# Performance work log

Measured on AMD Instinct MI355X. Metric: run time of the kernel, lower is better.

The kernel has to match this reference:

```python
import jax, jax.numpy as jnp
import numpy as np

VOCAB = 32000
EMBED = 512
HIDDEN = 512
SEQ = 4096


def setup_inputs() -> dict:
    key = jax.random.key(0)
    ks = jax.random.split(key, 20)
    s = 1.0 / np.sqrt(HIDDEN)

    def n(k, shape):
        return (jax.random.normal(k, shape, dtype=jnp.float32) * s).astype(jnp.float32)

    inp = {}
    inp["input"] = jax.random.randint(ks[0], (SEQ,), 0, VOCAB)
    inp["embed_w"] = n(ks[1], (VOCAB, EMBED))
    # layer 0 (input size EMBED), forward and backward directions; gate order i,f,g,o
    inp["Wih0f"] = n(ks[2], (4 * HIDDEN, EMBED))
    inp["Whh0f"] = n(ks[3], (4 * HIDDEN, HIDDEN))
    inp["b0f"] = n(ks[4], (4 * HIDDEN,))  # b_ih + b_hh combined (same math)
    inp["Wih0b"] = n(ks[5], (4 * HIDDEN, EMBED))
    inp["Whh0b"] = n(ks[6], (4 * HIDDEN, HIDDEN))
    inp["b0b"] = n(ks[7], (4 * HIDDEN,))
    # layer 1 (input size 2*HIDDEN)
    inp["Wih1f"] = n(ks[8], (4 * HIDDEN, 2 * HIDDEN))
    inp["Whh1f"] = n(ks[9], (4 * HIDDEN, HIDDEN))
    inp["b1f"] = n(ks[10], (4 * HIDDEN,))
    inp["Wih1b"] = n(ks[11], (4 * HIDDEN, 2 * HIDDEN))
    inp["Whh1b"] = n(ks[12], (4 * HIDDEN, HIDDEN))
    inp["b1b"] = n(ks[13], (4 * HIDDEN,))
    # output head
    inp["Wlin"] = n(ks[14], (VOCAB, 2 * HIDDEN))
    inp["blin"] = n(ks[15], (VOCAB,))
    return inp


def _lstm_dir(xproj, Whh, reverse):
    # xproj: [S, 4H] = x @ Wih.T + b, precomputed outside the scan.
    H = Whh.shape[1]
    WhhT = Whh.T  # [H, 4H]

    def step(carry, xp):
        h, c = carry
        g = xp + h @ WhhT  # [4H]
        i, f, gg, o = jnp.split(g, 4)
        i = jax.nn.sigmoid(i)
        f = jax.nn.sigmoid(f)
        gg = jnp.tanh(gg)
        o = jax.nn.sigmoid(o)
        c = f * c + i * gg
        h = o * jnp.tanh(c)
        return (h, c), h

    h0 = jnp.zeros((H,), xproj.dtype)
    _, hs = jax.lax.scan(step, (h0, h0), xproj, reverse=reverse)
    return hs  # [S, H], aligned to original time order


def _bilstm_layer(x, Wihf, Whhf, bf, Wihb, Whhb, bb):
    hf = _lstm_dir(x @ Wihf.T + bf, Whhf, reverse=False)
    hb = _lstm_dir(x @ Wihb.T + bb, Whhb, reverse=True)
    return jnp.concatenate([hf, hb], axis=-1)  # [S, 2H]


def reference(input, embed_w, Wih0f, Whh0f, b0f, Wih0b, Whh0b, b0b,
              Wih1f, Whh1f, b1f, Wih1b, Whh1b, b1b, Wlin, blin):
    x = embed_w[input]  # [S, E]  (batch=1 squeezed away; same math)
    x = _bilstm_layer(x, Wih0f, Whh0f, b0f, Wih0b, Whh0b, b0b)
    x = _bilstm_layer(x, Wih1f, Whh1f, b1f, Wih1b, Whh1b, b1b)
    out = x @ Wlin.T + blin  # [S, VOCAB]
    return out
```

## Files before the change

### kernel.cpp

```cpp
#include <hip/hip_runtime.h>
#include <hip/hip_bf16.h>
#include <stdint.h>

#define S_LEN 4096

typedef __attribute__((ext_vector_type(8))) short short8;
typedef __attribute__((ext_vector_type(4))) float f32x4;

__device__ inline unsigned short f2bf(float f) {
  unsigned int x = __float_as_uint(f);
  x += 0x7fffu + ((x >> 16) & 1u);
  return (unsigned short)(x >> 16);
}

__device__ inline float sigm(float x) { return 1.0f / (1.0f + __expf(-x)); }
__device__ inline float tanhf_(float x) {
  float e = __expf(-2.0f * fabsf(x));
  float t = (1.0f - e) / (1.0f + e);
  return copysignf(t, x);
}

__device__ inline void gload_lds16(const void* g, void* l) {
  __builtin_amdgcn_global_load_lds(
      (const __attribute__((address_space(1))) unsigned int*)g,
      (__attribute__((address_space(3))) unsigned int*)l, 16, 0, 0);
}

__global__ void embed_kernel(const int* __restrict__ idx, const float* __restrict__ E,
                             unsigned short* __restrict__ x0b) {
  const int row = blockIdx.x;
  const int t = threadIdx.x;
  const int id = idx[row];
  f32x4 v = ((const f32x4*)(E + (size_t)id * 512))[t];
  ushort4 u;
  u.x = f2bf(v[0]); u.y = f2bf(v[1]); u.z = f2bf(v[2]); u.w = f2bf(v[3]);
  ((ushort4*)(x0b + (size_t)row * 512))[t] = u;
}

__global__ void f32_to_bf16_kernel(const float* __restrict__ src, unsigned short* __restrict__ dst) {
  const size_t i = (size_t)blockIdx.x * blockDim.x + threadIdx.x;
  f32x4 v = ((const f32x4*)src)[i];
  ushort4 u;
  u.x = f2bf(v[0]); u.y = f2bf(v[1]); u.z = f2bf(v[2]); u.w = f2bf(v[3]);
  ((ushort4*)dst)[i] = u;
}

template <bool BF32>
__global__ __launch_bounds__(256) void gemm_bt(
    const unsigned short* __restrict__ A,
    const void* __restrict__ Bsrc,
    const float* __restrict__ bias,
    float* __restrict__ C,
    int M, int N, int K)
{
  __shared__ unsigned short Al[128 * 32];
  __shared__ unsigned short Bl[128 * 32];
  const int tiles_n = N >> 7;
  const int tm = (blockIdx.x / tiles_n) << 7;
  const int tn = (blockIdx.x % tiles_n) << 7;
  const int t = threadIdx.x;
  const int w = t >> 6, l = t & 63;
  const int wr = w >> 1, wc = w & 1;

  f32x4 acc[4][4] = {};

  for (int k0 = 0; k0 < K; k0 += 32) {
    __syncthreads();
    {
      const int rb = w * 32;
      const unsigned short* ga = A + (size_t)(tm + rb + (l >> 2)) * K + k0 + (l & 3) * 8;
      gload_lds16(ga, &Al[rb * 32]);
      gload_lds16(ga + (size_t)16 * K, &Al[(rb + 16) * 32]);
    }
    if constexpr (!BF32) {
      const unsigned short* B = (const unsigned short*)Bsrc;
      const int rb = w * 32;
      const unsigned short* gb = B + (size_t)(tn + rb + (l >> 2)) * K + k0 + (l & 3) * 8;
      gload_lds16(gb, &Bl[rb * 32]);
      gload_lds16(gb + (size_t)16 * K, &Bl[(rb + 16) * 32]);
    } else {
      const float* B = (const float*)Bsrc;
      const int row = t >> 1, half = t & 1;
      const f32x4* src = (const f32x4*)(B + (size_t)(tn + row) * K + k0 + half * 16);
      f32x4 v0 = src[0], v1 = src[1], v2 = src[2], v3 = src[3];
      short8 p0, p1;
      p0[0] = f2bf(v0[0]); p0[1] = f2bf(v0[1]); p0[2] = f2bf(v0[2]); p0[3] = f2bf(v0[3]);
      p0[4] = f2bf(v1[0]); p0[5] = f2bf(v1[1]); p0[6] = f2bf(v1[2]); p0[7] = f2bf(v1[3]);
      p1[0] = f2bf(v2[0]); p1[1] = f2bf(v2[1]); p1[2] = f2bf(v2[2]); p1[3] = f2bf(v2[3]);
      p1[4] = f2bf(v3[0]); p1[5] = f2bf(v3[1]); p1[6] = f2bf(v3[2]); p1[7] = f2bf(v3[3]);
      *(short8*)&Bl[row * 32 + half * 16] = p0;
      *(short8*)&Bl[row * 32 + half * 16 + 8] = p1;
    }
    __syncthreads();

    const int lrow = l & 15;
    const int lkb = (l >> 4) * 8;
    short8 af[4], bfr[4];
    #pragma unroll
    for (int fm = 0; fm < 4; fm++)
      af[fm] = *(const short8*)&Al[(wr * 64 + fm * 16 + lrow) * 32 + lkb];
    #pragma unroll
    for (int fn = 0; fn < 4; fn++)
      bfr[fn] = *(const short8*)&Bl[(wc * 64 + fn * 16 + lrow) * 32 + lkb];
    #pragma unroll
    for (int fm = 0; fm < 4; fm++)
      #pragma unroll
      for (int fn = 0; fn < 4; fn++)
        acc[fm][fn] = __builtin_amdgcn_mfma_f32_16x16x32_bf16(af[fm], bfr[fn], acc[fm][fn], 0, 0, 0);
  }

  const int r0 = tm + wr * 64;
  const int c0 = tn + wc * 64 + (l & 15);
  const int rbase = (l >> 4) * 4;
  #pragma unroll
  for (int fm = 0; fm < 4; fm++) {
    #pragma unroll
    for (int fn = 0; fn < 4; fn++) {
      const int col = c0 + fn * 16;
      const float bv = bias ? bias[col] : 0.0f;
      #pragma unroll
      for (int rg = 0; rg < 4; rg++) {
        const int rr = r0 + fm * 16 + rbase + rg;
        C[(size_t)rr * N + col] = acc[fm][fn][rg] + bv;
      }
    }
  }
}

__global__ __launch_bounds__(512, 1) void lstm_layer(
    const float* __restrict__ WhhF, const float* __restrict__ WhhB,
    const float* __restrict__ biasF, const float* __restrict__ biasB,
    const float* __restrict__ xproj,
    unsigned int* __restrict__ Hx,
    unsigned short* __restrict__ Hb)
{
  const int S = S_LEN;
  const int dir = blockIdx.x & 1;
  const int chunk = blockIdx.x >> 1;
  const float* Whh = dir ? WhhB : WhhF;
  const float* bias = dir ? biasB : biasF;
  const int t = threadIdx.x;
  const int w = t >> 6, l = t & 63;
  const int g = l >> 4;
  const int jl = (l >> 3) & 1;
  const int o = l & 7;
  const int elem = w * 2 + jl;
  const int r = g * 512 + chunk * 16 + elem;
  const int xoff = dir * 2048, hoff = dir * 512;

  f32x4 wv[16];
  {
    const f32x4* wp = (const f32x4*)(Whh + (size_t)r * 512 + o * 64);
    #pragma unroll
    for (int i = 0; i < 16; i++) {
      asm volatile("global_load_dwordx4 %0, %1, off\n\ts_waitcnt vmcnt(0)"
                   : "=v"(wv[i]) : "v"(wp + i) : "memory");
    }
  }
  const float bv = bias[r];

  __shared__ float hsh[2][8 * 68];
  float c = 0.0f;
  const int slot = (t >> 6) * 68 + (t & 63);

  float xp_cur = 0.0f;
  if (o == 0) {
    const int t0 = dir ? (S - 1) : 0;
    xp_cur = xproj[(size_t)t0 * 4096 + xoff + r] + bv;
  }

  for (int st = 0; st < S; st++) {
    const int tcur = dir ? (S - 1 - st) : st;
    const int pp = st & 1;

    float xp_nxt = 0.0f;
    if (o == 0 && st + 1 < S) {
      const int tn = dir ? (S - 2 - st) : (st + 1);
      xp_nxt = xproj[(size_t)tn * 4096 + xoff + r] + bv;
    }

    if (st == 0) {
      hsh[0][slot] = 0.0f;
    } else {
      const int tprev = dir ? (tcur + 1) : (tcur - 1);
      const unsigned int* src = Hx + (size_t)tprev * 1024 + hoff + t;
      unsigned int v;
      int cap = 1 << 16;
      do {
        v = __hip_atomic_load(src, __ATOMIC_RELAXED, __HIP_MEMORY_SCOPE_AGENT);
      } while (v == 0xFFFFFFFFu && --cap > 0);
      hsh[pp][slot] = __uint_as_float(v);
    }
    __syncthreads();

    float acc = 0.0f;
    const f32x4* hp = (const f32x4*)&hsh[pp][o * 68];
    #pragma unroll
    for (int i = 0; i < 16; i++) {
      f32x4 h4 = hp[i];
      acc = fmaf(wv[i][0], h4[0], acc);
      acc = fmaf(wv[i][1], h4[1], acc);
      acc = fmaf(wv[i][2], h4[2], acc);
      acc = fmaf(wv[i][3], h4[3], acc);
    }
    acc += __shfl_xor(acc, 1);
    acc += __shfl_xor(acc, 2);
    acc += __shfl_xor(acc, 4);
    acc += xp_cur;

    const float av = (g == 2) ? tanhf_(acc) : sigm(acc);
    const float f_ = __shfl(av, (l & 8) + 16);
    const float g_ = __shfl(av, (l & 8) + 32);
    const float o_ = __shfl(av, (l & 8) + 48);

    if ((l & 55) == 0) {
      c = f_ * c + av * g_;
      const float h = o_ * tanhf_(c);
      const size_t ofs = (size_t)tcur * 1024 + hoff + chunk * 16 + elem;
      __hip_atomic_store(Hx + ofs, __float_as_uint(h),
                         __ATOMIC_RELAXED, __HIP_MEMORY_SCOPE_AGENT);
      Hb[ofs] = f2bf(h);
    }
    xp_cur = xp_nxt;
  }
}

extern "C" void kernel_launch(void* const* d_in, const int* in_sizes, int n_in,
                              void* d_out, int out_size, void* d_ws, size_t ws_size,
                              hipStream_t stream) {
  (void)in_sizes; (void)n_in; (void)out_size; (void)ws_size;
  const int*   input   = (const int*)d_in[0];
  const float* embed_w = (const float*)d_in[1];
  const float* Wih0f   = (const float*)d_in[2];
  const float* Whh0f   = (const float*)d_in[3];
  const float* b0f     = (const float*)d_in[4];
  const float* Wih0b   = (const float*)d_in[5];
  const float* Whh0b   = (const float*)d_in[6];
  const float* b0b     = (const float*)d_in[7];
  const float* Wih1f   = (const float*)d_in[8];
  const float* Whh1f   = (const float*)d_in[9];
  const float* b1f     = (const float*)d_in[10];
  const float* Wih1b   = (const float*)d_in[11];
  const float* Whh1b   = (const float*)d_in[12];
  const float* b1b     = (const float*)d_in[13];
  const float* Wlin    = (const float*)d_in[14];
  const float* blin    = (const float*)d_in[15];

  char* ws = (char*)d_ws;
  unsigned short* x0b   = (unsigned short*)(ws);
  unsigned short* Wih0  = (unsigned short*)(ws + ((size_t)4  << 20));
  unsigned short* Wih1  = (unsigned short*)(ws + ((size_t)8  << 20));
  unsigned short* H0b   = (unsigned short*)(ws + ((size_t)16 << 20));
  unsigned short* H1b   = (unsigned short*)(ws + ((size_t)24 << 20));

  float* dout  = (float*)d_out;
  float* xproj = dout;
  unsigned int* H0 = (unsigned int*)(dout + ((size_t)16 << 20));
  unsigned int* H1 = (unsigned int*)(dout + ((size_t)20 << 20));

  hipMemsetAsync(H0, 0xFF, (size_t)8 * 1024 * 1024 * 4, stream);

  embed_kernel<<<4096, 128, 0, stream>>>(input, embed_w, x0b);

  f32_to_bf16_kernel<<<1024, 256, 0, stream>>>(Wih0f, Wih0);
  f32_to_bf16_kernel<<<1024, 256, 0, stream>>>(Wih0b, Wih0 + (size_t)2048 * 512);
  f32_to_bf16_kernel<<<2048, 256, 0, stream>>>(Wih1f, Wih1);
  f32_to_bf16_kernel<<<2048, 256, 0, stream>>>(Wih1b, Wih1 + (size_t)2048 * 1024);

  gemm_bt<false><<<32 * 32, 256, 0, stream>>>(x0b, Wih0, nullptr, xproj, 4096, 4096, 512);
  lstm_layer<<<64, 512, 0, stream>>>(Whh0f, Whh0b, b0f, b0b, xproj, H0, H0b);

  gemm_bt<false><<<32 * 32, 256, 0, stream>>>(H0b, Wih1, nullptr, xproj, 4096, 4096, 1024);
  lstm_layer<<<64, 512, 0, stream>>>(Whh1f, Whh1b, b1f, b1b, xproj, H1, H1b);

  gemm_bt<true><<<32 * 250, 256, 0, stream>>>(H1b, Wlin, blin, dout, 4096, 32000, 1024);
}
```

Baseline: 12.00 ms.

## Stream bf16 recurrent weights from cache each step and pack h exchanges into 64-bit words

Recurrent weights are converted to bf16 once up front, and the LSTM kernel now reloads them from global memory/cache on every timestep instead of holding 64 fp32 values per thread in registers. The hidden-state exchange between blocks uses 64-bit atomic loads and stores covering two elements, which halves the polling and store traffic, and every lane now computes the cell update. This cuts register pressure but adds a per-step weight reload on the serial recurrence path and lowers the precision of the recurrent weights.

```diff
diff --git a/kernel.cpp b/kernel.cpp
--- a/kernel.cpp
+++ b/kernel.cpp
@@ -5,12 +5,17 @@
 #define S_LEN 4096
 
 typedef __attribute__((ext_vector_type(8))) short short8;
+typedef __attribute__((ext_vector_type(8))) unsigned short ushort8;
 typedef __attribute__((ext_vector_type(4))) float f32x4;
+typedef __attribute__((ext_vector_type(2))) float f32x2;
 
 __device__ inline unsigned short f2bf(float f) {
   unsigned int x = __float_as_uint(f);
   x += 0x7fffu + ((x >> 16) & 1u);
   return (unsigned short)(x >> 16);
+}
+__device__ inline float bf2f(unsigned short u) {
+  return __uint_as_float(((unsigned int)u) << 16);
 }
 
 __device__ inline float sigm(float x) { return 1.0f / (1.0f + __expf(-x)); }
@@ -128,7 +133,8 @@
 }
 
 __global__ __launch_bounds__(512, 1) void lstm_layer(
-    const float* __restrict__ WhhF, const float* __restrict__ WhhB,
+    const unsigned short* __restrict__ WhhBf16F,
+    const unsigned short* __restrict__ WhhBf16B,
     const float* __restrict__ biasF, const float* __restrict__ biasB,
     const float* __restrict__ xproj,
     unsigned int* __restrict__ Hx,
@@ -137,7 +143,7 @@
   const int S = S_LEN;
   const int dir = blockIdx.x & 1;
   const int chunk = blockIdx.x >> 1;
-  const float* Whh = dir ? WhhB : WhhF;
+  const unsigned short* Whh = dir ? WhhBf16B : WhhBf16F;
   const float* bias = dir ? biasB : biasF;
   const int t = threadIdx.x;
   const int w = t >> 6, l = t & 63;
@@ -148,20 +154,12 @@
   const int r = g * 512 + chunk * 16 + elem;
   const int xoff = dir * 2048, hoff = dir * 512;
 
-  f32x4 wv[16];
-  {
-    const f32x4* wp = (const f32x4*)(Whh + (size_t)r * 512 + o * 64);
-    #pragma unroll
-    for (int i = 0; i < 16; i++) {
-      asm volatile("global_load_dwordx4 %0, %1, off\n\ts_waitcnt vmcnt(0)"
-                   : "=v"(wv[i]) : "v"(wp + i) : "memory");
-    }
-  }
+  const ushort8* wp = (const ushort8*)(Whh + (size_t)r * 512 + o * 64);
   const float bv = bias[r];
 
   __shared__ float hsh[2][8 * 68];
   float c = 0.0f;
-  const int slot = (t >> 6) * 68 + (t & 63);
+  const int slot2 = (t >> 5) * 68 + ((2 * t) & 63);
 
   float xp_cur = 0.0f;
   if (o == 0) {
@@ -173,6 +171,10 @@
     const int tcur = dir ? (S - 1 - st) : st;
     const int pp = st & 1;
 
+    ushort8 wv[8];
+    #pragma unroll
+    for (int j = 0; j < 8; j++) wv[j] = wp[j];
+
     float xp_nxt = 0.0f;
     if (o == 0 && st + 1 < S) {
       const int tn = dir ? (S - 2 - st) : (st + 1);
@@ -180,28 +182,32 @@
     }
 
     if (st == 0) {
-      hsh[0][slot] = 0.0f;
-    } else {
+      if (t < 256) *(f32x2*)&hsh[0][slot2] = f32x2{0.0f, 0.0f};
+    } else if (t < 256) {
       const int tprev = dir ? (tcur + 1) : (tcur - 1);
-      const unsigned int* src = Hx + (size_t)tprev * 1024 + hoff + t;
-      unsigned int v;
+      const unsigned long long* src =
+          (const unsigned long long*)(Hx + (size_t)tprev * 1024 + hoff) + t;
+      unsigned long long v;
       int cap = 1 << 16;
       do {
         v = __hip_atomic_load(src, __ATOMIC_RELAXED, __HIP_MEMORY_SCOPE_AGENT);
-      } while (v == 0xFFFFFFFFu && --cap > 0);
-      hsh[pp][slot] = __uint_as_float(v);
+      } while (((v >> 32) == 0xFFFFFFFFull || (v & 0xFFFFFFFFull) == 0xFFFFFFFFull)
+               && --cap > 0);
+      *(f32x2*)&hsh[pp][slot2] =
+          f32x2{__uint_as_float((unsigned int)v), __uint_as_float((unsigned int)(v >> 32))};
     }
     __syncthreads();
 
     float acc = 0.0f;
-    const f32x4* hp = (const f32x4*)&hsh[pp][o * 68];
+    const float* hb = &hsh[pp][o * 68];
     #pragma unroll
     for (int i = 0; i < 16; i++) {
-      f32x4 h4 = hp[i];
-      acc = fmaf(wv[i][0], h4[0], acc);
-      acc = fmaf(wv[i][1], h4[1], acc);
-      acc = fmaf(wv[i][2], h4[2], acc);
-      acc = fmaf(wv[i][3], h4[3], acc);
+      f32x4 h4 = *(const f32x4*)&hb[4 * i];
+      const int j = i >> 1, hf = (i & 1) * 4;
+      acc = fmaf(bf2f(wv[j][hf + 0]), h4[0], acc);
+      acc = fmaf(bf2f(wv[j][hf + 1]), h4[1], acc);
+      acc = fmaf(bf2f(wv[j][hf + 2]), h4[2], acc);
+      acc = fmaf(bf2f(wv[j][hf + 3]), h4[3], acc);
     }
     acc += __shfl_xor(acc, 1);
     acc += __shfl_xor(acc, 2);
@@ -213,13 +219,19 @@
     const float g_ = __shfl(av, (l & 8) + 32);
     const float o_ = __shfl(av, (l & 8) + 48);
 
-    if ((l & 55) == 0) {
-      c = f_ * c + av * g_;
-      const float h = o_ * tanhf_(c);
-      const size_t ofs = (size_t)tcur * 1024 + hoff + chunk * 16 + elem;
-      __hip_atomic_store(Hx + ofs, __float_as_uint(h),
+    c = f_ * c + av * g_;
+    const float h = o_ * tanhf_(c);
+    const float hpair = __shfl(h, 8);
+
+    if (l == 0) {
+      const size_t eofs = (size_t)tcur * 1024 + hoff + chunk * 16 + 2 * w;
+      const unsigned long long pk =
+          (unsigned long long)__float_as_uint(h) |
+          ((unsigned long long)__float_as_uint(hpair) << 32);
+      __hip_atomic_store((unsigned long long*)(Hx + eofs), pk,
                          __ATOMIC_RELAXED, __HIP_MEMORY_SCOPE_AGENT);
-      Hb[ofs] = f2bf(h);
+      const unsigned int hb2 = (unsigned int)f2bf(h) | ((unsigned int)f2bf(hpair) << 16);
+      *(unsigned int*)(Hb + eofs) = hb2;
     }
     xp_cur = xp_nxt;
   }
@@ -257,6 +269,11 @@
   float* xproj = dout;
   unsigned int* H0 = (unsigned int*)(dout + ((size_t)16 << 20));
   unsigned int* H1 = (unsigned int*)(dout + ((size_t)20 << 20));
+  unsigned short* WhhB = (unsigned short*)(dout + ((size_t)24 << 20));
+  unsigned short* Whh0fb = WhhB;
+  unsigned short* Whh0bb = WhhB + ((size_t)1 << 20);
+  unsigned short* Whh1fb = WhhB + ((size_t)2 << 20);
+  unsigned short* Whh1bb = WhhB + ((size_t)3 << 20);
 
   hipMemsetAsync(H0, 0xFF, (size_t)8 * 1024 * 1024 * 4, stream);
 
@@ -266,12 +283,16 @@
   f32_to_bf16_kernel<<<1024, 256, 0, stream>>>(Wih0b, Wih0 + (size_t)2048 * 512);
   f32_to_bf16_kernel<<<2048, 256, 0, stream>>>(Wih1f, Wih1);
   f32_to_bf16_kernel<<<2048, 256, 0, stream>>>(Wih1b, Wih1 + (size_t)2048 * 1024);
+  f32_to_bf16_kernel<<<1024, 256, 0, stream>>>(Whh0f, Whh0fb);
+  f32_to_bf16_kernel<<<1024, 256, 0, stream>>>(Whh0b, Whh0bb);
+  f32_to_bf16_kernel<<<1024, 256, 0, stream>>>(Whh1f, Whh1fb);
+  f32_to_bf16_kernel<<<1024, 256, 0, stream>>>(Whh1b, Whh1bb);
 
   gemm_bt<false><<<32 * 32, 256, 0, stream>>>(x0b, Wih0, nullptr, xproj, 4096, 4096, 512);
-  lstm_layer<<<64, 512, 0, stream>>>(Whh0f, Whh0b, b0f, b0b, xproj, H0, H0b);
+  lstm_layer<<<64, 512, 0, stream>>>(Whh0fb, Whh0bb, b0f, b0b, xproj, H0, H0b);
 
   gemm_bt<false><<<32 * 32, 256, 0, stream>>>(H0b, Wih1, nullptr, xproj, 4096, 4096, 1024);
-  lstm_layer<<<64, 512, 0, stream>>>(Whh1f, Whh1b, b1f, b1b, xproj, H1, H1b);
+  lstm_layer<<<64, 512, 0, stream>>>(Whh1fb, Whh1bb, b1f, b1b, xproj, H1, H1b);
 
   gemm_bt<true><<<32 * 250, 256, 0, stream>>>(H1b, Wlin, blin, dout, 4096, 32000, 1024);
 }
```

After: 12.38 ms. +3.2%, slower.
